# Kernel tuning notes

Measured on AMD Instinct MI355X. Metric: run time of the kernel, lower is better.

Reference implementation:

```python
import jax, jax.numpy as jnp
import numpy as np

BETA = 0.25      # commitment loss weight
JSD_TS = 1.0     # softmax temperature


def _pairwise_sq_dist(x, cb):
    return (jnp.sum(x * x, axis=1, keepdims=True)
            + jnp.sum(cb * cb, axis=1)
            - 2.0 * jnp.matmul(x, cb.T))


def setup_inputs() -> dict:
    key = jax.random.key(0)
    k1, k2, k3 = jax.random.split(key, 3)
    B, D, H, W, K = 8, 512, 64, 64, 1024
    z = jax.random.normal(k1, (B, D, H, W), dtype=jnp.float32)
    z_pos = jax.random.normal(k2, (B, D, H, W), dtype=jnp.float32)
    # matches embedding.weight.data.uniform_(-1/K, 1/K)
    codebook = jax.random.uniform(k3, (K, D), dtype=jnp.float32,
                                  minval=-1.0 / K, maxval=1.0 / K)
    return {"z": z, "z_pos": z_pos, "codebook": codebook}


def reference(z, z_pos, codebook):
    b, d, h, w = z.shape
    # (b, d, h, w) -> (bhw, d)
    z_flat = jnp.transpose(z, (0, 2, 3, 1)).reshape(-1, d)
    z_pos_flat = jnp.transpose(z_pos, (0, 2, 3, 1)).reshape(-1, d)

    # normalize == 'none': z_norm = z_flat, codebook_norm = codebook
    dist = _pairwise_sq_dist(z_flat, codebook)          # (n, K)
    pos_dist = _pairwise_sq_dist(z_pos_flat, codebook)  # (n, K)

    min_encoding_indices = jnp.argmin(dist, axis=1)     # (n,)
    distance_prob = jax.nn.softmax(-dist / JSD_TS, axis=1)
    pos_distance_prob = jax.nn.softmax(-pos_dist / JSD_TS, axis=1)

    # use_weighted_sum == False: gather codebook rows
    z_q = codebook[min_encoding_indices]                # (n, d)

    codebook_loss = jnp.mean((z_q - jax.lax.stop_gradient(z_flat)) ** 2)
    commitment_loss = jnp.mean((z_flat - jax.lax.stop_gradient(z_q)) ** 2)
    q_loss = codebook_loss + BETA * commitment_loss

    # straight-through estimator
    z_q = z_flat + jax.lax.stop_gradient(z_q - z_flat)

    z_q = jnp.transpose(z_q.reshape(b, h, w, d), (0, 3, 1, 2))  # (b, d, h, w)
    return (z_q,
            q_loss,
            distance_prob.reshape(b, h, w, -1),
            min_encoding_indices.reshape(b, h, w),
            pos_distance_prob.reshape(b, h, w, -1))
```

## Files before the change

### kernel.cpp

```cpp
#include <hip/hip_runtime.h>
#include <hip/hip_bf16.h>

static constexpr int Bn = 8, Dn = 512, Hn = 64, Wn = 64, Kn = 1024;
static constexpr int HW = Hn * Wn;
static constexpr int NPIX = Bn * HW;
static constexpr size_t OFF_LOSS = (size_t)Bn * Dn * HW;
static constexpr size_t OFF_PROB = OFF_LOSS + 1;
static constexpr size_t OFF_IDX  = OFF_PROB + (size_t)NPIX * Kn;
static constexpr size_t OFF_PPRB = OFF_IDX + NPIX;

typedef __attribute__((ext_vector_type(8))) short short8v;
typedef __attribute__((ext_vector_type(4))) float f32x4;
typedef unsigned long long ull;
typedef unsigned int uint32;

static constexpr size_t WS_CB2   = 0;
static constexpr size_t WS_XXZ   = 4096;
static constexpr size_t WS_WIDX  = 135168;
static constexpr size_t WS_PART  = 266240;
static constexpr size_t WS_CBBF  = 282624;
static constexpr size_t WS_ABF   = 1331200;
static constexpr size_t ABF_BYTES = (size_t)2 * NPIX * Dn * 2;

#define MARGIN 1e-3f
#define CANDSLACK 2.5e-3f

__device__ inline unsigned short f2bf(float x) {
  unsigned u = __float_as_uint(x);
  u += 0x7fffu + ((u >> 16) & 1u);
  return (unsigned short)(u >> 16);
}
__device__ inline unsigned pack2(float a, float b) {
  return (unsigned)f2bf(a) | ((unsigned)f2bf(b) << 16);
}
__device__ inline float bf2f(unsigned short h) {
  return __uint_as_float(((unsigned)h) << 16);
}

__device__ inline void gload_lds16(const void* g, void* l) {
  __builtin_amdgcn_global_load_lds((const __attribute__((address_space(1))) void*)g,
                                   (__attribute__((address_space(3))) void*)l, 16, 0, 0);
}

__device__ float np_pairwise_sq512(const float* __restrict__ base, int stride) {
  float B[4];
#pragma unroll
  for (int blk = 0; blk < 4; blk++) {
    const float* a = base + (size_t)blk * 128 * stride;
    float r[8][4];
#pragma unroll
    for (int k = 0; k < 8; k++)
#pragma unroll
      for (int j = 0; j < 4; j++) {
        float x = a[(size_t)(4 * k + j) * stride];
        r[k][j] = __fmul_rn(x, x);
      }
#pragma unroll
    for (int i = 32; i < 128; i += 32)
#pragma unroll
      for (int k = 0; k < 8; k++)
#pragma unroll
        for (int j = 0; j < 4; j++) {
          float x = a[(size_t)(i + 4 * k + j) * stride];
          r[k][j] = __fadd_rn(r[k][j], __fmul_rn(x, x));
        }
    float L[4];
#pragma unroll
    for (int j = 0; j < 4; j++) {
      float t01 = __fadd_rn(r[0][j], r[1][j]);
      float t23 = __fadd_rn(r[2][j], r[3][j]);
      float t45 = __fadd_rn(r[4][j], r[5][j]);
      float t67 = __fadd_rn(r[6][j], r[7][j]);
      L[j] = __fadd_rn(__fadd_rn(t01, t23), __fadd_rn(t45, t67));
    }
    B[blk] = __fadd_rn(__fadd_rn(L[0], L[1]), __fadd_rn(L[2], L[3]));
  }
  return __fadd_rn(__fadd_rn(B[0], B[1]), __fadd_rn(B[2], B[3]));
}

__global__ __launch_bounds__(256) void k_init(const float* __restrict__ Z,
                                              const float* __restrict__ ZP,
                                              const float* __restrict__ CB,
                                              unsigned short* __restrict__ CBbf,
                                              unsigned short* __restrict__ Abf,
                                              float* __restrict__ xxZ,
                                              float* __restrict__ cb2) {
  int gid = blockIdx.x * 256 + threadIdx.x;
  {
    float2 f = *(const float2*)(CB + (size_t)gid * 2);
    union { __hip_bfloat162 h; unsigned u; } cv;
    cv.h = __float22bfloat162_rn(f);
    ((unsigned*)CBbf)[gid] = cv.u;
  }
  if (gid < 2 * NPIX) {
    const int p = gid & (NPIX - 1);
    const bool isz = gid < NPIX;
    const float* src = (isz ? Z : ZP) + (size_t)(p >> 12) * (Dn * HW) + (p & 4095);
    unsigned short* dst = Abf + (size_t)gid * Dn;
    float Bb[4];
#pragma unroll
    for (int blk = 0; blk < 4; blk++) {
      float rr[32];
#pragma unroll
      for (int i = 0; i < 128; i += 32) {
        float v[32];
#pragma unroll
        for (int t = 0; t < 32; t++) v[t] = src[(size_t)(blk * 128 + i + t) * HW];
        uint4 ua;
        unsigned* uw = (unsigned*)&ua;
#pragma unroll
        for (int q = 0; q < 4; q++) {
#pragma unroll
          for (int e = 0; e < 4; e++) uw[e] = pack2(v[q * 8 + 2 * e], v[q * 8 + 2 * e + 1]);
          *(uint4*)&dst[blk * 128 + i + q * 8] = ua;
        }
        if (isz) {
          if (i == 0) {
#pragma unroll
            for (int t = 0; t < 32; t++) rr[t] = __fmul_rn(v[t], v[t]);
          } else {
#pragma unroll
            for (int t = 0; t < 32; t++) rr[t] = __fadd_rn(rr[t], __fmul_rn(v[t], v[t]));
          }
        }
      }
      if (isz) {
        float L[4];
#pragma unroll
        for (int j = 0; j < 4; j++) {
          float t01 = __fadd_rn(rr[0 + j], rr[4 + j]);
          float t23 = __fadd_rn(rr[8 + j], rr[12 + j]);
          float t45 = __fadd_rn(rr[16 + j], rr[20 + j]);
          float t67 = __fadd_rn(rr[24 + j], rr[28 + j]);
          L[j] = __fadd_rn(__fadd_rn(t01, t23), __fadd_rn(t45, t67));
        }
        Bb[blk] = __fadd_rn(__fadd_rn(L[0], L[1]), __fadd_rn(L[2], L[3]));
      }
    }
    if (isz)
      xxZ[p] = __fadd_rn(__fadd_rn(Bb[0], Bb[1]), __fadd_rn(Bb[2], Bb[3]));
  } else if (gid < 2 * NPIX + Kn) {
    int k = gid - 2 * NPIX;
    cb2[k] = np_pairwise_sq512(CB + (size_t)k * Dn, 1);
  }
}

__global__ __launch_bounds__(256) void k_gemm(const unsigned short* __restrict__ Abf,
                                              const unsigned short* __restrict__ CBbf,
                                              const float* __restrict__ cb2,
                                              float* __restrict__ out) {
  __shared__ __align__(16) unsigned short sE[16384];
  __shared__ float c2s[128];
  __shared__ float rsv[2][128][2];
  __shared__ int   rsi[2][128];

  const int bid = blockIdx.x;
  const int kx = (bid >> 3) & 7;
  const int panel = (bid & 7) + 8 * (bid >> 6);
  const int py = panel & 255;
  const int zz = panel >> 8;
  const int p0 = py * 128;
  const int k0 = kx * 128;
  const unsigned short* Asrc = Abf + (size_t)((zz ? NPIX : 0) + p0) * Dn;
  float* Sf = out + (zz ? OFF_PPRB : OFF_PROB);
  uint32* Sg = (uint32*)Sf;

  const int tid = threadIdx.x;
  const int lane = tid & 63, w = tid >> 6;
  const int fr = lane & 15, fg = lane >> 4;
  const int wm = w & 1, wn = w >> 1;
  if (tid < 128) c2s[tid] = cb2[k0 + tid];

  auto stage = [&](int buf, int c0) {
#pragma unroll
    for (int h = 0; h < 2; h++) {
      const int G = tid + h * 256;
      const int row = G >> 2, g = G & 3;
      const int gsrc = g ^ ((row >> 1) & 3);
      const int ldsbase = ((tid & 192) + h * 256) * 8;
      gload_lds16(Asrc + (size_t)row * Dn + c0 + gsrc * 8, &sE[buf * 4096 + ldsbase]);
      gload_lds16(CBbf + (size_t)(k0 + row) * Dn + c0 + gsrc * 8,
                  &sE[8192 + buf * 4096 + ldsbase]);
    }
  };

  stage(0, 0);
  f32x4 acc[4][4] = {};
  const int swz = (fr >> 1) & 3;
#pragma unroll
  for (int s = 0; s < 16; s++) {
    __syncthreads();
    if (s < 15) stage((s + 1) & 1, (s + 1) * 32);
    const int cur = s & 1;
    short8v kf[4], pf[4];
#pragma unroll
    for (int m = 0; m < 4; m++)
      kf[m] = *(const short8v*)&sE[8192 + cur * 4096 + (wm * 64 + m * 16 + fr) * 32 + ((fg ^ swz) * 8)];
#pragma unroll
    for (int n = 0; n < 4; n++)
      pf[n] = *(const short8v*)&sE[cur * 4096 + (wn * 64 + n * 16 + fr) * 32 + ((fg ^ swz) * 8)];
#pragma unroll
    for (int m = 0; m < 4; m++)
#pragma unroll
      for (int n = 0; n < 4; n++)
        acc[m][n] = __builtin_amdgcn_mfma_f32_16x16x32_bf16(kf[m], pf[n], acc[m][n], 0, 0, 0);
  }

  __syncthreads();
  float v1a[4], v2a[4];
  int i1a[4];
#pragma unroll
  for (int n = 0; n < 4; n++) { v1a[n] = 1e30f; v2a[n] = 1e30f; i1a[n] = 0x7fffffff; }
#pragma unroll
  for (int m = 0; m < 4; m++) {
    const int kkb = wm * 64 + m * 16 + fg * 4;
    const float4 c2v = *(const float4*)&c2s[kkb];
#pragma unroll
    for (int n = 0; n < 4; n++) {
      const int px = wn * 64 + n * 16 + fr;
      float s0 = __fsub_rn(c2v.x, __fmul_rn(2.0f, acc[m][n][0]));
      float s1 = __fsub_rn(c2v.y, __fmul_rn(2.0f, acc[m][n][1]));
      float s2 = __fsub_rn(c2v.z, __fmul_rn(2.0f, acc[m][n][2]));
      float s3 = __fsub_rn(c2v.w, __fmul_rn(2.0f, acc[m][n][3]));
      uint2 pk;
      pk.x = pack2(s0, s1);
      pk.y = pack2(s2, s3);
      *(uint2*)((char*)sE + px * 256 + ((kkb * 2) ^ ((px & 15) << 4))) = pk;
      if (s0 < v1a[n]) { v2a[n] = v1a[n]; v1a[n] = s0; i1a[n] = kkb; }
      else if (s0 < v2a[n]) v2a[n] = s0;
      if (s1 < v1a[n]) { v2a[n] = v1a[n]; v1a[n] = s1; i1a[n] = kkb + 1; }
      else if (s1 < v2a[n]) v2a[n] = s1;
      if (s2 < v1a[n]) { v2a[n] = v1a[n]; v1a[n] = s2; i1a[n] = kkb + 2; }
      else if (s2 < v2a[n]) v2a[n] = s2;
      if (s3 < v1a[n]) { v2a[n] = v1a[n]; v1a[n] = s3; i1a[n] = kkb + 3; }
      else if (s3 < v2a[n]) v2a[n] = s3;
    }
  }
#pragma unroll
  for (int n = 0; n < 4; n++) {
    float v1 = v1a[n], v2 = v2a[n];
    int i1 = i1a[n];
#pragma unroll
    for (int d = 16; d < 64; d <<= 1) {
      float ov1 = __shfl_xor(v1, d, 64);
      int oi1 = __shfl_xor(i1, d, 64);
      float ov2 = __shfl_xor(v2, d, 64);
      float lose;
      if (ov1 < v1 || (ov1 == v1 && oi1 < i1)) { lose = v1; v1 = ov1; i1 = oi1; }
      else lose = ov1;
      v2 = fminf(fminf(v2, ov2), lose);
    }
    if (fg == 0) {
      const int px = wn * 64 + n * 16 + fr;
      rsv[wm][px][0] = v1; rsv[wm][px][1] = v2; rsi[wm][px] = i1;
    }
  }
  __syncthreads();

  if (zz == 0 && tid < 128) {
    float v1 = rsv[0][tid][0], v2 = rsv[0][tid][1];
    int i1 = rsi[0][tid];
    float ov1 = rsv[1][tid][0], ov2 = rsv[1][tid][1];
    int oi1 = rsi[1][tid];
    float lose;
    if (ov1 < v1 || (ov1 == v1 && oi1 < i1)) { lose = v1; v1 = ov1; i1 = oi1; }
    else lose = ov1;
    v2 = fminf(fminf(v2, ov2), lose);
    float4 st;
    st.x = v1; st.y = v2; st.z = __int_as_float(k0 + i1); st.w = 0.f;
    *(float4*)(Sf + (size_t)(p0 + tid) * Kn + 512 + kx * 4) = st;
  }

  const int rr = tid >> 5;
  const int c32 = tid & 31;
#pragma unroll
  for (int pass = 0; pass < 16; pass++) {
    const int px = pass * 8 + rr;
    uint32* dst = Sg + (size_t)(p0 + px) * Kn + kx * 64;
#pragma unroll
    for (int i = 0; i < 2; i++) {
      const int w32 = c32 + 32 * i;
      dst[w32] = *(const uint32*)((const char*)sE + px * 256 + ((w32 * 4) ^ ((px & 15) << 4)));
    }
  }
}

__global__ __launch_bounds__(256) void k_row(const float* __restrict__ Z,
                                             const float* __restrict__ CB,
                                             const float* __restrict__ cb2,
                                             const float* __restrict__ xxZ,
                                             float* __restrict__ out,
                                             int* __restrict__ widx,
                                             float* __restrict__ partial) {
  __shared__ float lsum[4];
  const int zz = blockIdx.y;
  const int p0 = blockIdx.x * 16;
  float* Sbase = out + (zz ? OFF_PPRB : OFF_PROB);
  const int tid = threadIdx.x;
  const int lane = tid & 63, w = tid >> 6;
  float wloss = 0.f;

#pragma unroll 1
  for (int i = 0; i < 4; i++) {
    const int p = p0 + w * 4 + i;
    float* Sp = Sbase + (size_t)p * Kn;
    const uint32* Su = (const uint32*)Sp;
    uint32 uv[8];
#pragma unroll
    for (int q = 0; q < 8; q++) uv[q] = Su[q * 64 + lane];

    float sv[16];
    float sum = 0.f;
#pragma unroll
    for (int q = 0; q < 8; q++) {
      float s0 = bf2f((unsigned short)uv[q]);
      float s1 = bf2f((unsigned short)(uv[q] >> 16));
      sv[2 * q] = s0; sv[2 * q + 1] = s1;
      sum += __expf(-s0) + __expf(-s1);
    }
#pragma unroll
    for (int d = 1; d < 64; d <<= 1) sum += __shfl_xor(sum, d, 64);
    const float inv = 1.0f / sum;

    float v1 = 1e30f, v2 = 1e30f;
    int i1 = 0x7fffffff;
    if (zz == 0) {
      if (lane < 8) {
        float4 st = ((const float4*)(Sp + 512))[lane];
        v1 = st.x; v2 = st.y; i1 = __float_as_int(st.z);
      }
#pragma unroll
      for (int d = 1; d < 8; d <<= 1) {
        float ov1 = __shfl_xor(v1, d, 64);
        int oi1 = __shfl_xor(i1, d, 64);
        float ov2 = __shfl_xor(v2, d, 64);
        float lose;
        if (ov1 < v1 || (ov1 == v1 && oi1 < i1)) { lose = v1; v1 = ov1; i1 = oi1; }
        else lose = ov1;
        v2 = fminf(fminf(v2, ov2), lose);
      }
      v1 = __shfl(v1, 0, 64);
      v2 = __shfl(v2, 0, 64);
      i1 = __shfl(i1, 0, 64);
    }

#pragma unroll
    for (int q = 0; q < 8; q++) {
      int k0 = (q * 64 + lane) * 2;
      Sp[k0] = __expf(-sv[2 * q]) * inv;
      Sp[k0 + 1] = __expf(-sv[2 * q + 1]) * inv;
    }

    if (zz == 0) {
      int fin = i1;
      float dfin = v1;
      if (v2 <= v1 + MARGIN) {
        const float thrc = v1 + CANDSLACK;
        const float* zcol = Z + (size_t)(p >> 12) * (Dn * HW) + (p & 4095);
        float zc[8];
#pragma unroll
        for (int q = 0; q < 8; q++) zc[q] = zcol[(size_t)(lane + 64 * q) * HW];
        const float xx = xxZ[p];
        float bd = 1e30f;
        int bi = 0x7fffffff;
#pragma unroll
        for (int q = 0; q < 8; q++) {
#pragma unroll
          for (int hi = 0; hi < 2; hi++) {
            ull mask = __ballot(sv[2 * q + hi] <= thrc);
            while (mask) {
              int l = __ffsll(mask) - 1;
              mask &= mask - 1;
              int k = (q * 64 + l) * 2 + hi;
              const float* cr = CB + (size_t)k * Dn;
              float part = 0.f;
#pragma unroll
              for (int q2 = 0; q2 < 8; q2++)
                part = fmaf(zc[q2], cr[lane + 64 * q2], part);
#pragma unroll
              for (int d = 1; d < 64; d <<= 1) part += __shfl_xor(part, d, 64);
              float dd = __fsub_rn(__fadd_rn(xx, cb2[k]), __fmul_rn(2.0f, part));
              if (dd < bd || (dd == bd && k < bi)) { bd = dd; bi = k; }
            }
          }
        }
        fin = bi;
        dfin = bd - xx;
      }
      wloss += xxZ[p] + dfin;
      if (lane == 0) {
        widx[p] = fin;
        out[OFF_IDX + p] = (float)fin;
      }
    }
  }
  if (zz == 0) {
    if (lane == 0) lsum[w] = wloss;
    __syncthreads();
    if (tid == 0)
      partial[blockIdx.x] = (lsum[0] + lsum[1]) + (lsum[2] + lsum[3]);
  }
}

__global__ __launch_bounds__(256) void k_zq(const float* __restrict__ CB,
                                            const int* __restrict__ widx,
                                            float* __restrict__ out) {
  __shared__ float tile[64][65];
  __shared__ int wl[64];
  const int p0 = blockIdx.x * 64;
  const int b = p0 >> 12, hw0 = p0 & 4095;
  const int tid = threadIdx.x;
  if (tid < 64) wl[tid] = widx[p0 + tid];
  __syncthreads();
  const int px = tid >> 2, q = tid & 3;
  const int px2 = tid & 63, cg = tid >> 6;
  float* obase = out + (size_t)b * (Dn * HW) + hw0;
  for (int c0 = 0; c0 < 512; c0 += 64) {
    const float4* src = (const float4*)(CB + (size_t)wl[px] * Dn + c0 + q * 16);
#pragma unroll
    for (int j = 0; j < 4; j++) {
      float4 v = src[j];
      int c = q * 16 + j * 4;
      tile[c + 0][px] = v.x; tile[c + 1][px] = v.y;
      tile[c + 2][px] = v.z; tile[c + 3][px] = v.w;
    }
    __syncthreads();
#pragma unroll
    for (int pass = 0; pass < 16; pass++) {
      int c = pass * 4 + cg;
      obase[(size_t)(c0 + c) * HW + px2] = tile[c][px2];
    }
    __syncthreads();
  }
}

__global__ __launch_bounds__(256) void k_loss(const float* __restrict__ partial,
                                              float* __restrict__ out) {
  __shared__ float red[256];
  const int t = threadIdx.x;
  float s = 0.f;
  for (int i = t; i < 2048; i += 256) s += partial[i];
  red[t] = s;
  __syncthreads();
  for (int k = 128; k > 0; k >>= 1) {
    if (t < k) red[t] += red[t + k];
    __syncthreads();
  }
  if (t == 0) out[OFF_LOSS] = red[0] * (1.25f / 16777216.0f);
}

extern "C" void kernel_launch(void* const* d_in, const int* in_sizes, int n_in,
                              void* d_out, int out_size, void* d_ws, size_t ws_size,
                              hipStream_t stream) {
  const float* Z = (const float*)d_in[0];
  const float* ZP = (const float*)d_in[1];
  const float* CB = (const float*)d_in[2];
  float* out = (float*)d_out;
  char* ws = (char*)d_ws;
  float* cb2 = (float*)(ws + WS_CB2);
  float* xxZ = (float*)(ws + WS_XXZ);
  int* widx = (int*)(ws + WS_WIDX);
  float* partial = (float*)(ws + WS_PART);
  unsigned short* CBbf = (unsigned short*)(ws + WS_CBBF);
  unsigned short* Abf = (ws_size >= WS_ABF + ABF_BYTES)
                            ? (unsigned short*)(ws + WS_ABF)
                            : (unsigned short*)d_out;

  k_init<<<dim3(1024), 256, 0, stream>>>(Z, ZP, CB, CBbf, Abf, xxZ, cb2);
  k_gemm<<<dim3(4096), 256, 0, stream>>>(Abf, CBbf, cb2, out);
  k_row<<<dim3(2048, 2), 256, 0, stream>>>(Z, CB, cb2, xxZ, out, widx, partial);
  k_zq<<<dim3(512), 256, 0, stream>>>(CB, widx, out);
  k_loss<<<dim3(1), 256, 0, stream>>>(partial, out);
}
```

Before: 355.1 us.

## Triple-buffer GEMM LDS staging with vmcnt-based waits and single barrier

The bf16 distance GEMM moves from a double-buffered LDS pipeline to a three-stage ring. Loads run two K-steps ahead, and synchronisation uses explicit s_waitcnt vmcnt plus a raw s_barrier instead of __syncthreads at the top of each step. The aim is to hide global-to-LDS load latency behind the MFMA work and cut the barrier stall per step. In exchange, LDS use per block rises from 32 KB to 48 KB, which may lower occupancy. The gain is also limited because the large probability output writes likely dominate the runtime.

```diff
diff --git a/kernel.cpp b/kernel.cpp
--- a/kernel.cpp
+++ b/kernel.cpp
@@ -149,7 +149,7 @@
                                               const unsigned short* __restrict__ CBbf,
                                               const float* __restrict__ cb2,
                                               float* __restrict__ out) {
-  __shared__ __align__(16) unsigned short sE[16384];
+  __shared__ __align__(16) unsigned short sE[24576];
   __shared__ float c2s[128];
   __shared__ float rsv[2][128][2];
   __shared__ int   rsi[2][128];
@@ -171,39 +171,55 @@
   const int wm = w & 1, wn = w >> 1;
   if (tid < 128) c2s[tid] = cb2[k0 + tid];
 
-  auto stage = [&](int buf, int c0) {
+  auto stage = [&](int t) {
+    const int buf = t % 3;
+    const int c0 = t * 32;
 #pragma unroll
     for (int h = 0; h < 2; h++) {
       const int G = tid + h * 256;
       const int row = G >> 2, g = G & 3;
       const int gsrc = g ^ ((row >> 1) & 3);
-      const int ldsbase = ((tid & 192) + h * 256) * 8;
+      const int ldsbase = (tid & 192) * 8 + h * 2048;
       gload_lds16(Asrc + (size_t)row * Dn + c0 + gsrc * 8, &sE[buf * 4096 + ldsbase]);
       gload_lds16(CBbf + (size_t)(k0 + row) * Dn + c0 + gsrc * 8,
-                  &sE[8192 + buf * 4096 + ldsbase]);
+                  &sE[12288 + buf * 4096 + ldsbase]);
     }
   };
 
-  stage(0, 0);
+  stage(0);
+  stage(1);
+  asm volatile("s_waitcnt vmcnt(4)" ::: "memory");
+  __builtin_amdgcn_s_barrier();
+  __builtin_amdgcn_sched_barrier(0);
+
   f32x4 acc[4][4] = {};
   const int swz = (fr >> 1) & 3;
 #pragma unroll
   for (int s = 0; s < 16; s++) {
-    __syncthreads();
-    if (s < 15) stage((s + 1) & 1, (s + 1) * 32);
-    const int cur = s & 1;
+    if (s < 14) stage(s + 2);
+    const int buf = s % 3;
     short8v kf[4], pf[4];
 #pragma unroll
     for (int m = 0; m < 4; m++)
-      kf[m] = *(const short8v*)&sE[8192 + cur * 4096 + (wm * 64 + m * 16 + fr) * 32 + ((fg ^ swz) * 8)];
+      kf[m] = *(const short8v*)&sE[12288 + buf * 4096 + (wm * 64 + m * 16 + fr) * 32 + ((fg ^ swz) * 8)];
 #pragma unroll
     for (int n = 0; n < 4; n++)
-      pf[n] = *(const short8v*)&sE[cur * 4096 + (wn * 64 + n * 16 + fr) * 32 + ((fg ^ swz) * 8)];
+      pf[n] = *(const short8v*)&sE[buf * 4096 + (wn * 64 + n * 16 + fr) * 32 + ((fg ^ swz) * 8)];
 #pragma unroll
     for (int m = 0; m < 4; m++)
 #pragma unroll
       for (int n = 0; n < 4; n++)
         acc[m][n] = __builtin_amdgcn_mfma_f32_16x16x32_bf16(kf[m], pf[n], acc[m][n], 0, 0, 0);
+    if (s < 15) {
+      __builtin_amdgcn_sched_barrier(0);
+      if (s < 14) {
+        asm volatile("s_waitcnt vmcnt(4)" ::: "memory");
+      } else {
+        asm volatile("s_waitcnt vmcnt(0)" ::: "memory");
+      }
+      __builtin_amdgcn_s_barrier();
+      __builtin_amdgcn_sched_barrier(0);
+    }
   }
 
   __syncthreads();
```

Result: faster. 347.9 us (-2.0%).
